# Performance work log

Measured on AMD Instinct MI355X. Metric: run time of the kernel, lower is better.

## Reference

```python
import jax, jax.numpy as jnp
import numpy as np

V, E, H, LM, LC = 50257, 512, 1024, 128, 256


def gru_cell(x, h, Wih, Whh, bih, bhh):
    # PyTorch nn.GRU cell, gate order (r, z, n)
    gi = x @ Wih.T + bih
    gh = h @ Whh.T + bhh
    i_r, i_z, i_n = jnp.split(gi, 3, -1)
    h_r, h_z, h_n = jnp.split(gh, 3, -1)
    r = jax.nn.sigmoid(i_r + h_r)
    z = jax.nn.sigmoid(i_z + h_z)
    n = jnp.tanh(i_n + r * h_n)
    return (1.0 - z) * n + z * h


def setup_inputs() -> dict:
    key = jax.random.key(0)
    ks = jax.random.split(key, 18)
    f = lambda k, sh: jax.random.normal(k, sh, jnp.float32) * 0.02
    return {
        "motion": jax.random.randint(ks[0], (1, LM), 0, V),
        "target_output": jax.random.randint(ks[1], (1, LC), 0, V),
        "enc_emb": f(ks[2], (V, E)),
        "enc_Wih": f(ks[3], (3 * H, E)),
        "enc_Whh": f(ks[4], (3 * H, H)),
        "enc_bih": f(ks[5], (3 * H,)),
        "enc_bhh": f(ks[6], (3 * H,)),
        "dec_emb": f(ks[7], (V, H)),
        "dec_Wih": f(ks[8], (3 * H, H)),
        "dec_Whh": f(ks[9], (3 * H, H)),
        "dec_bih": f(ks[10], (3 * H,)),
        "dec_bhh": f(ks[11], (3 * H,)),
        "attn_W": f(ks[12], (LM, 2 * H)),
        "attn_b": f(ks[13], (LM,)),
        "comb_W": f(ks[14], (H, 2 * H)),
        "comb_b": f(ks[15], (H,)),
        "out_W": f(ks[16], (V, H)),
        "out_b": f(ks[17], (V,)),
    }


def reference(motion, target_output, enc_emb, enc_Wih, enc_Whh, enc_bih, enc_bhh,
              dec_emb, dec_Wih, dec_Whh, dec_bih, dec_bhh,
              attn_W, attn_b, comb_W, comb_b, out_W, out_b):
    # ----- encode: per-step GRU over motion tokens (batch is hard-coded 1) -----
    toks = motion[0]  # [LM]

    def enc_step(h, t):
        h2 = gru_cell(enc_emb[t], h, enc_Wih, enc_Whh, enc_bih, enc_bhh)
        return h2, h2

    h0 = jnp.zeros((H,), jnp.float32)
    enc_h, enc_outs = jax.lax.scan(enc_step, h0, toks)  # enc_outs: [LM, H]

    # ----- decode with teacher forcing -----
    # original: decoder_input = SOS at idx 0, then target[idx-1] set at end of
    # step idx => step idx+1 consumes target[idx-1]; step 1 consumes target[-1].
    tgt = target_output[0]  # [LC]
    dec_in = jnp.concatenate([jnp.zeros((1,), tgt.dtype), tgt[-1:], tgt[:-2]])  # [LC]

    def dec_step(h, t):
        emb = dec_emb[t]  # [H] (dropout is identity at inference)
        attn_w = jax.nn.softmax(jnp.concatenate([emb, h]) @ attn_W.T + attn_b)  # [LM]
        ctx = attn_w @ enc_outs  # [H]
        x = jnp.concatenate([emb, ctx]) @ comb_W.T + comb_b  # [H] (no relu in source)
        h2 = gru_cell(x, h, dec_Wih, dec_Whh, dec_bih, dec_bhh)
        logp = jax.nn.log_softmax(h2 @ out_W.T + out_b)  # [V]
        return h2, logp

    _, logps = jax.lax.scan(dec_step, enc_h, dec_in)  # [LC, V]
    return logps[None]  # [1, LC, V] (permute(1,0,2) with batch=1)
```

## Files before the change

### kernel.cpp

```cpp
#include <hip/hip_runtime.h>

#define V_ 50257
#define E_ 512
#define H_ 1024
#define LM_ 128
#define LC_ 256
#define NBLK 256
#define ROWS 12
#define AREP 16
#define HREP 8
#define NT_OUT 786

typedef __attribute__((ext_vector_type(8))) short short8;
typedef __attribute__((ext_vector_type(4))) float f32x4;
typedef unsigned long long u64;

__device__ __forceinline__ unsigned short f2bf(float x) {
  union { float f; unsigned u; } v; v.f = x;
  unsigned r = v.u + 0x7fffu + ((v.u >> 16) & 1u);
  return (unsigned short)(r >> 16);
}
__device__ __forceinline__ float bflo(unsigned u) { union { unsigned u; float f; } v; v.u = u << 16; return v.f; }
__device__ __forceinline__ float bfhi(unsigned u) { union { unsigned u; float f; } v; v.u = u & 0xffff0000u; return v.f; }

__device__ __forceinline__ int grow4(int s, int i0) {
  return (s < 4) ? (i0 + s) : (s < 8) ? (1024 + i0 + (s - 4)) : (2048 + i0 + (s - 8));
}

__device__ __forceinline__ void st_u32(unsigned* p, unsigned v) {
  __hip_atomic_store(p, v, __ATOMIC_RELAXED, __HIP_MEMORY_SCOPE_AGENT);
}
__device__ __forceinline__ void st_u64(u64* p, u64 v) {
  __hip_atomic_store(p, v, __ATOMIC_RELAXED, __HIP_MEMORY_SCOPE_AGENT);
}
__device__ __forceinline__ u64 ld_u64(const u64* p) {
  return __hip_atomic_load(p, __ATOMIC_RELAXED, __HIP_MEMORY_SCOPE_AGENT);
}
__device__ __forceinline__ unsigned ld_u32(const unsigned* p) {
  return __hip_atomic_load(p, __ATOMIC_RELAXED, __HIP_MEMORY_SCOPE_AGENT);
}
__device__ __forceinline__ void atom_add_f32(float* p, float v) {
  (void)__hip_atomic_fetch_add(p, v, __ATOMIC_RELAXED, __HIP_MEMORY_SCOPE_AGENT);
}

__global__ void build_dec_tok(const int* __restrict__ tgt, int* __restrict__ dtok) {
  int t = threadIdx.x;
  dtok[t] = (t == 0) ? 0 : (t == 1 ? tgt[LC_ - 1] : tgt[t - 2]);
}

__global__ __launch_bounds__(256) void gemm_g(const float* __restrict__ A, int lda,
                                              const int* __restrict__ ridx,
                                              const float* __restrict__ B, int ldb,
                                              const float* __restrict__ bias,
                                              float* __restrict__ C, int ldc, int K) {
  __shared__ float As[16][68];
  __shared__ float Bs[16][68];
  const int bm = blockIdx.y * 64, bn = blockIdx.x * 64;
  const int tid = threadIdx.x;
  const int tx = tid & 15, ty = tid >> 4;
  const int lm = tid & 63, lk = (tid >> 6) * 4;
  const int arow = ridx ? ridx[bm + lm] : (bm + lm);
  const float* Arow = A + (size_t)arow * lda;
  float acc[4][4] = {};
  for (int k0 = 0; k0 < K; k0 += 16) {
    float4 av = *(const float4*)&Arow[k0 + lk];
    float4 bv = *(const float4*)&B[(size_t)(bn + lm) * ldb + k0 + lk];
    As[lk + 0][lm] = av.x; As[lk + 1][lm] = av.y; As[lk + 2][lm] = av.z; As[lk + 3][lm] = av.w;
    Bs[lk + 0][lm] = bv.x; Bs[lk + 1][lm] = bv.y; Bs[lk + 2][lm] = bv.z; Bs[lk + 3][lm] = bv.w;
    __syncthreads();
#pragma unroll
    for (int kk = 0; kk < 16; ++kk) {
      float4 a4 = *(const float4*)&As[kk][ty * 4];
      float4 b4 = *(const float4*)&Bs[kk][tx * 4];
      acc[0][0] += a4.x * b4.x; acc[0][1] += a4.x * b4.y; acc[0][2] += a4.x * b4.z; acc[0][3] += a4.x * b4.w;
      acc[1][0] += a4.y * b4.x; acc[1][1] += a4.y * b4.y; acc[1][2] += a4.y * b4.z; acc[1][3] += a4.y * b4.w;
      acc[2][0] += a4.z * b4.x; acc[2][1] += a4.z * b4.y; acc[2][2] += a4.z * b4.z; acc[2][3] += a4.z * b4.w;
      acc[3][0] += a4.w * b4.x; acc[3][1] += a4.w * b4.y; acc[3][2] += a4.w * b4.z; acc[3][3] += a4.w * b4.w;
    }
    __syncthreads();
  }
#pragma unroll
  for (int i = 0; i < 4; ++i) {
#pragma unroll
    for (int j = 0; j < 4; ++j) {
      int gm = bm + ty * 4 + i, gn = bn + tx * 4 + j;
      float bv = bias ? bias[gn] : 0.f;
      C[(size_t)gm * ldc + gn] = acc[i][j] + bv;
    }
  }
}

__global__ __launch_bounds__(256) void gemm_dual(const float* __restrict__ A, int lda,
                                                 const int* __restrict__ ridx,
                                                 const float* __restrict__ combW,
                                                 const float* __restrict__ comb_b,
                                                 const float* __restrict__ attnW,
                                                 const float* __restrict__ attn_b,
                                                 float* __restrict__ xE,
                                                 float* __restrict__ aE, int K) {
  __shared__ float As[16][68];
  __shared__ float Bs[16][68];
  const int bm = blockIdx.y * 64;
  const bool is_x = blockIdx.x < 16;
  const int bn = (is_x ? blockIdx.x : (blockIdx.x - 16)) * 64;
  const float* B = is_x ? combW : attnW;
  const int ldb = 2048;
  const float* bias = is_x ? comb_b : attn_b;
  float* C = is_x ? xE : aE;
  const int ldc = is_x ? 1024 : 128;
  const int tid = threadIdx.x;
  const int tx = tid & 15, ty = tid >> 4;
  const int lm = tid & 63, lk = (tid >> 6) * 4;
  const int arow = ridx[bm + lm];
  const float* Arow = A + (size_t)arow * lda;
  float acc[4][4] = {};
  for (int k0 = 0; k0 < K; k0 += 16) {
    float4 av = *(const float4*)&Arow[k0 + lk];
    float4 bv = *(const float4*)&B[(size_t)(bn + lm) * ldb + k0 + lk];
    As[lk + 0][lm] = av.x; As[lk + 1][lm] = av.y; As[lk + 2][lm] = av.z; As[lk + 3][lm] = av.w;
    Bs[lk + 0][lm] = bv.x; Bs[lk + 1][lm] = bv.y; Bs[lk + 2][lm] = bv.z; Bs[lk + 3][lm] = bv.w;
    __syncthreads();
#pragma unroll
    for (int kk = 0; kk < 16; ++kk) {
      float4 a4 = *(const float4*)&As[kk][ty * 4];
      float4 b4 = *(const float4*)&Bs[kk][tx * 4];
      acc[0][0] += a4.x * b4.x; acc[0][1] += a4.x * b4.y; acc[0][2] += a4.x * b4.z; acc[0][3] += a4.x * b4.w;
      acc[1][0] += a4.y * b4.x; acc[1][1] += a4.y * b4.y; acc[1][2] += a4.y * b4.z; acc[1][3] += a4.y * b4.w;
      acc[2][0] += a4.z * b4.x; acc[2][1] += a4.z * b4.y; acc[2][2] += a4.z * b4.z; acc[2][3] += a4.z * b4.w;
      acc[3][0] += a4.w * b4.x; acc[3][1] += a4.w * b4.y; acc[3][2] += a4.w * b4.z; acc[3][3] += a4.w * b4.w;
    }
    __syncthreads();
  }
#pragma unroll
  for (int i = 0; i < 4; ++i) {
#pragma unroll
    for (int j = 0; j < 4; ++j) {
      int gm = bm + ty * 4 + i, gn = bn + tx * 4 + j;
      C[(size_t)gm * ldc + gn] = acc[i][j] + bias[gn];
    }
  }
}

__global__ __launch_bounds__(256) void enc_rnn(const float* __restrict__ Whh,
                                               const float* __restrict__ bhh,
                                               const float* __restrict__ gi,
                                               u64* __restrict__ epk,
                                               float* __restrict__ outs) {
  __shared__ unsigned short Whl[ROWS][1024];
  __shared__ unsigned h_sh[512];
  __shared__ float h_own[4];
  __shared__ float bh[ROWS];
  __shared__ float ghl[ROWS];
  const int b = blockIdx.x, tid = threadIdx.x;
  const int w = tid >> 6, l = tid & 63;
  const int i0 = b * 4;
  const u64* myrep = epk + (size_t)(b & (HREP - 1)) * 1024;
  for (int idx = tid; idx < ROWS * 1024; idx += 256) {
    int s = idx >> 10, c = idx & 1023;
    Whl[s][c] = f2bf(Whh[(size_t)grow4(s, i0) * H_ + c]);
  }
  if (tid < ROWS) bh[tid] = bhh[grow4(tid, i0)];
  if (tid < 4) h_own[tid] = 0.f;
  __syncthreads();

  for (int t = 0; t < LM_; ++t) {
    float gr = 0.f, gz = 0.f, gn_ = 0.f;
    if (tid < 4) {
      const float* git = gi + (size_t)t * 3072;
      gr = git[i0 + tid]; gz = git[1024 + i0 + tid]; gn_ = git[2048 + i0 + tid];
    }
    if (t == 0) {
      h_sh[2 * tid] = 0u; h_sh[2 * tid + 1] = 0u;
    } else {
      const u64* pb = myrep + (size_t)(t & 1) * 512 + 2 * tid;
      const unsigned g = (unsigned)t;
      u64 q0, q1;
      for (;;) {
        q0 = ld_u64(pb); q1 = ld_u64(pb + 1);
        if ((unsigned)(q0 >> 32) == g && (unsigned)(q1 >> 32) == g) break;
        __builtin_amdgcn_s_sleep(1);
      }
      h_sh[2 * tid] = (unsigned)q0;
      h_sh[2 * tid + 1] = (unsigned)q1;
    }
    __syncthreads();

    for (int s = w; s < ROWS; s += 4) {
      float acc = 0.f;
#pragma unroll
      for (int e = 0; e < 8; ++e) {
        unsigned u = *(const unsigned*)&Whl[s][2 * (e * 64 + l)];
        unsigned hv = h_sh[e * 64 + l];
        acc += bflo(u) * bflo(hv) + bfhi(u) * bfhi(hv);
      }
#pragma unroll
      for (int off = 32; off; off >>= 1) acc += __shfl_xor(acc, off);
      if (l == 0) ghl[s] = acc;
    }
    __syncthreads();
    if (tid < 4) {
      int i = tid, ig = i0 + i;
      float hr = ghl[i] + bh[i], hz = ghl[4 + i] + bh[4 + i], hn = ghl[8 + i] + bh[8 + i];
      float r = 1.f / (1.f + expf(-(gr + hr)));
      float z = 1.f / (1.f + expf(-(gz + hz)));
      float n = tanhf(gn_ + r * hn);
      float hpv = (1.f - z) * n + z * h_own[i];
      h_own[i] = hpv;
      float v0 = __shfl(hpv, 0), v1 = __shfl(hpv, 1);
      float v2 = __shfl(hpv, 2), v3 = __shfl(hpv, 3);
      if (tid == 0) {
        u64 gg = (u64)(unsigned)(t + 1) << 32;
        u64 p0 = gg | (u64)((unsigned)f2bf(v0) | ((unsigned)f2bf(v1) << 16));
        u64 p1 = gg | (u64)((unsigned)f2bf(v2) | ((unsigned)f2bf(v3) << 16));
        size_t slot = (size_t)((t + 1) & 1) * 512 + 2 * b;
#pragma unroll
        for (int r2 = 0; r2 < HREP; ++r2) {
          st_u64(epk + (size_t)r2 * 1024 + slot, p0);
          st_u64(epk + (size_t)r2 * 1024 + slot + 1, p1);
        }
      }
      outs[(size_t)t * H_ + ig] = hpv;
    }
  }
}

__global__ __launch_bounds__(256) void dec_rnn(const float* __restrict__ Whh,
                                               const float* __restrict__ bhh,
                                               const float* __restrict__ attn_W,
                                               const float* __restrict__ G,
                                               const float* __restrict__ P1,
                                               const float* __restrict__ aE,
                                               const float* __restrict__ hfin,
                                               float* __restrict__ a_acc,
                                               u64* __restrict__ dpk,
                                               unsigned* __restrict__ dflags,
                                               unsigned short* __restrict__ Hs) {
  __shared__ unsigned short Whl[ROWS][1024];
  __shared__ unsigned Ac[2 * 128];
  __shared__ float Gl[ROWS][128];
  __shared__ unsigned h_sh[512];
  __shared__ float a_f[128];
  __shared__ float h_own[4];
  __shared__ float bh[ROWS];
  __shared__ float ghl[ROWS];
  __shared__ float giS[ROWS];
  const int b = blockIdx.x, tid = threadIdx.x;
  const int w = tid >> 6, l = tid & 63;
  const int i0 = b * 4;
  for (int idx = tid; idx < ROWS * 1024; idx += 256) {
    int s = idx >> 10, c = idx & 1023;
    Whl[s][c] = f2bf(Whh[(size_t)grow4(s, i0) * H_ + c]);
  }
  if (tid < 256) {
    int u = tid >> 7, j = tid & 127;
    float2 wv = *(const float2*)&attn_W[(size_t)j * 2048 + 1024 + i0 + 2 * u];
    Ac[tid] = (unsigned)f2bf(wv.x) | ((unsigned)f2bf(wv.y) << 16);
  }
  for (int idx = tid; idx < ROWS * 128; idx += 256) {
    int s = idx >> 7, c = idx & 127;
    Gl[s][c] = G[(size_t)grow4(s, i0) * 128 + c];
  }
  if (tid < ROWS) bh[tid] = bhh[grow4(tid, i0)];
  if (tid < 4) h_own[tid] = hfin[i0 + tid];
  __syncthreads();

  {
    float h0 = h_own[0], h1 = h_own[1], h2 = h_own[2], h3 = h_own[3];
    if (tid < 128) {
      unsigned w0 = Ac[tid], w1 = Ac[128 + tid];
      float a0 = bflo(w0) * h0 + bfhi(w0) * h1 + bflo(w1) * h2 + bfhi(w1) * h3;
      atom_add_f32(&a_acc[(b & (AREP - 1)) * 128 + tid], a0);
    }
    __syncthreads();
    if (tid == 0) st_u32(&dflags[b * 16], 1u);
  }

  for (int t = 0; t < LC_; ++t) {
    u64 aacc[16]; u64 aEv = 0;
    if (tid < 64) {
      const unsigned need = (unsigned)(t + 1);
      for (;;) {
        unsigned f0 = ld_u32(&dflags[tid * 16]);
        unsigned f1 = ld_u32(&dflags[(tid + 64) * 16]);
        unsigned f2 = ld_u32(&dflags[(tid + 128) * 16]);
        unsigned f3 = ld_u32(&dflags[(tid + 192) * 16]);
        unsigned mn = min(min(f0, f1), min(f2, f3));
        if (__all((int)(mn >= need))) break;
        __builtin_amdgcn_s_sleep(1);
      }
      const u64* ab = (const u64*)(a_acc + (size_t)t * (AREP * 128)) + l;
#pragma unroll
      for (int r = 0; r < AREP; ++r) aacc[r] = ld_u64(ab + r * 64);
      float2 ae2 = *(const float2*)&aE[(size_t)t * LM_ + 2 * l];
      aEv = ((u64)__float_as_uint(ae2.y) << 32) | (u64)__float_as_uint(ae2.x);
    }
    float p1p[3];
    if (l == 0) {
#pragma unroll
      for (int k = 0; k < 3; ++k) p1p[k] = P1[(size_t)t * 3072 + grow4(w + 4 * k, i0)];
    } else {
      p1p[0] = p1p[1] = p1p[2] = 0.f;
    }
    if (t == 0) {
      float4 hv = ((const float4*)hfin)[tid];
      h_sh[2 * tid] = (unsigned)f2bf(hv.x) | ((unsigned)f2bf(hv.y) << 16);
      h_sh[2 * tid + 1] = (unsigned)f2bf(hv.z) | ((unsigned)f2bf(hv.w) << 16);
    } else {
      const u64* pb = dpk + (size_t)(t & 1) * 512 + 2 * tid;
      const unsigned g = (unsigned)t;
      u64 q0, q1;
      for (;;) {
        q0 = ld_u64(pb); q1 = ld_u64(pb + 1);
        if ((unsigned)(q0 >> 32) == g && (unsigned)(q1 >> 32) == g) break;
        __builtin_amdgcn_s_sleep(1);
      }
      h_sh[2 * tid] = (unsigned)q0;
      h_sh[2 * tid + 1] = (unsigned)q1;
    }
    __syncthreads();

    if (tid < 64) {
      float s0 = 0.f, s1 = 0.f;
#pragma unroll
      for (int r = 0; r < AREP; ++r) {
        s0 += __uint_as_float((unsigned)aacc[r]);
        s1 += __uint_as_float((unsigned)(aacc[r] >> 32));
      }
      a_f[2 * l] = s0 + __uint_as_float((unsigned)aEv);
      a_f[2 * l + 1] = s1 + __uint_as_float((unsigned)(aEv >> 32));
    }
    for (int s = w; s < ROWS; s += 4) {
      float acc = 0.f;
#pragma unroll
      for (int e = 0; e < 8; ++e) {
        unsigned u = *(const unsigned*)&Whl[s][2 * (e * 64 + l)];
        unsigned hv = h_sh[e * 64 + l];
        acc += bflo(u) * bflo(hv) + bfhi(u) * bfhi(hv);
      }
#pragma unroll
      for (int off = 32; off; off >>= 1) acc += __shfl_xor(acc, off);
      if (l == 0) ghl[s] = acc;
    }
    __syncthreads();

    float ax = a_f[2 * l], ay = a_f[2 * l + 1];
    float mx = fmaxf(ax, ay);
#pragma unroll
    for (int off = 32; off; off >>= 1) mx = fmaxf(mx, __shfl_xor(mx, off));
    float pe0 = expf(ax - mx), pe1 = expf(ay - mx);
    float zs = pe0 + pe1;
#pragma unroll
    for (int off = 32; off; off >>= 1) zs += __shfl_xor(zs, off);
    float w0 = pe0 / zs, w1 = pe1 / zs;
#pragma unroll
    for (int k = 0; k < 3; ++k) {
      int s = w + 4 * k;
      float2 g2 = *(const float2*)&Gl[s][2 * l];
      float acc = g2.x * w0 + g2.y * w1;
#pragma unroll
      for (int off = 32; off; off >>= 1) acc += __shfl_xor(acc, off);
      if (l == 0) giS[s] = acc + p1p[k];
    }
    __syncthreads();

    if (tid < 4) {
      int i = tid, ig = i0 + i;
      float hr = ghl[i] + bh[i], hz = ghl[4 + i] + bh[4 + i], hn = ghl[8 + i] + bh[8 + i];
      float r = 1.f / (1.f + expf(-(giS[i] + hr)));
      float z = 1.f / (1.f + expf(-(giS[4 + i] + hz)));
      float n = tanhf(giS[8 + i] + r * hn);
      float hpv = (1.f - z) * n + z * h_own[i];
      h_own[i] = hpv;
      float v0 = __shfl(hpv, 0), v1 = __shfl(hpv, 1);
      float v2 = __shfl(hpv, 2), v3 = __shfl(hpv, 3);
      if (tid == 0 && t < LC_ - 1) {
        u64 gg = (u64)(unsigned)(t + 1) << 32;
        u64* pb = dpk + (size_t)((t + 1) & 1) * 512 + 2 * b;
        st_u64(pb,     gg | (u64)((unsigned)f2bf(v0) | ((unsigned)f2bf(v1) << 16)));
        st_u64(pb + 1, gg | (u64)((unsigned)f2bf(v2) | ((unsigned)f2bf(v3) << 16)));
      }
      Hs[(size_t)t * H_ + ig] = f2bf(hpv);
    }
    __syncthreads();

    if (t < LC_ - 1) {
      float h0 = h_own[0], h1 = h_own[1], h2 = h_own[2], h3 = h_own[3];
      if (tid < 128) {
        unsigned w0p = Ac[tid], w1p = Ac[128 + tid];
        float a0 = bflo(w0p) * h0 + bfhi(w0p) * h1 + bflo(w1p) * h2 + bfhi(w1p) * h3;
        atom_add_f32(&a_acc[(size_t)(t + 1) * (AREP * 128) + (b & (AREP - 1)) * 128 + tid], a0);
      }
    }
    __syncthreads();
    if (tid == 0) st_u32(&dflags[b * 16], (unsigned)(t + 2));
  }
}

__global__ __launch_bounds__(256) void out_gemm(const unsigned short* __restrict__ A,
                                                const float* __restrict__ Wf, int ldw,
                                                const float* __restrict__ bias,
                                                float* __restrict__ C,
                                                float* __restrict__ pmax,
                                                float* __restrict__ psum,
                                                int N, int K) {
  __shared__ unsigned short As[2][256][40];
  __shared__ unsigned short Bs[2][64][40];
  const int bn = blockIdx.x * 64, bx = blockIdx.x;
  const int tid = threadIdx.x, w = tid >> 6, l = tid & 63;
  const int NIT = K / 32;
  f32x4 acc[4][4];
#pragma unroll
  for (int mf = 0; mf < 4; ++mf)
#pragma unroll
    for (int nf = 0; nf < 4; ++nf) acc[mf][nf] = (f32x4){0.f, 0.f, 0.f, 0.f};

  const int bn_r0 = (tid) >> 3, bkc0 = tid & 7;
  const int bn_r1 = (tid + 256) >> 3, bkc1 = (tid + 256) & 7;

  short8 ar[4];
  float4 fv[2];
  {
    const unsigned short* src = A + (size_t)tid * K;
#pragma unroll
    for (int kc = 0; kc < 4; ++kc) ar[kc] = *(const short8*)(src + kc * 8);
    int gn0 = bn + bn_r0, gn1 = bn + bn_r1;
    fv[0] = (gn0 < N) ? *(const float4*)&Wf[(size_t)gn0 * ldw + bkc0 * 4] : (float4){0, 0, 0, 0};
    fv[1] = (gn1 < N) ? *(const float4*)&Wf[(size_t)gn1 * ldw + bkc1 * 4] : (float4){0, 0, 0, 0};
#pragma unroll
    for (int kc = 0; kc < 4; ++kc) *(short8*)&As[0][tid][kc * 8] = ar[kc];
    uint2 p0, p1;
    p0.x = (unsigned)f2bf(fv[0].x) | ((unsigned)f2bf(fv[0].y) << 16);
    p0.y = (unsigned)f2bf(fv[0].z) | ((unsigned)f2bf(fv[0].w) << 16);
    p1.x = (unsigned)f2bf(fv[1].x) | ((unsigned)f2bf(fv[1].y) << 16);
    p1.y = (unsigned)f2bf(fv[1].z) | ((unsigned)f2bf(fv[1].w) << 16);
    *(uint2*)&Bs[0][bn_r0][bkc0 * 4] = p0;
    *(uint2*)&Bs[0][bn_r1][bkc1 * 4] = p1;
  }

  for (int it = 0; it < NIT; ++it) {
    const int cur = it & 1, nxt = cur ^ 1;
    __syncthreads();
    if (it + 1 < NIT) {
      int k0n = (it + 1) * 32;
      const unsigned short* src = A + (size_t)tid * K + k0n;
#pragma unroll
      for (int kc = 0; kc < 4; ++kc) ar[kc] = *(const short8*)(src + kc * 8);
      int gn0 = bn + bn_r0, gn1 = bn + bn_r1;
      fv[0] = (gn0 < N) ? *(const float4*)&Wf[(size_t)gn0 * ldw + k0n + bkc0 * 4] : (float4){0, 0, 0, 0};
      fv[1] = (gn1 < N) ? *(const float4*)&Wf[(size_t)gn1 * ldw + k0n + bkc1 * 4] : (float4){0, 0, 0, 0};
    }
    const int k8 = (l >> 4) * 8;
    short8 af4[4], bf4[4];
#pragma unroll
    for (int mf = 0; mf < 4; ++mf) af4[mf] = *(const short8*)&As[cur][w * 64 + mf * 16 + (l & 15)][k8];
#pragma unroll
    for (int nf = 0; nf < 4; ++nf) bf4[nf] = *(const short8*)&Bs[cur][nf * 16 + (l & 15)][k8];
#pragma unroll
    for (int mf = 0; mf < 4; ++mf)
#pragma unroll
      for (int nf = 0; nf < 4; ++nf)
        acc[mf][nf] = __builtin_amdgcn_mfma_f32_16x16x32_bf16(af4[mf], bf4[nf], acc[mf][nf], 0, 0, 0);
    if (it + 1 < NIT) {
#pragma unroll
      for (int kc = 0; kc < 4; ++kc) *(short8*)&As[nxt][tid][kc * 8] = ar[kc];
      uint2 p0, p1;
      p0.x = (unsigned)f2bf(fv[0].x) | ((unsigned)f2bf(fv[0].y) << 16);
      p0.y = (unsigned)f2bf(fv[0].z) | ((unsigned)f2bf(fv[0].w) << 16);
      p1.x = (unsigned)f2bf(fv[1].x) | ((unsigned)f2bf(fv[1].y) << 16);
      p1.y = (unsigned)f2bf(fv[1].z) | ((unsigned)f2bf(fv[1].w) << 16);
      *(uint2*)&Bs[nxt][bn_r0][bkc0 * 4] = p0;
      *(uint2*)&Bs[nxt][bn_r1][bkc1 * 4] = p1;
    }
  }
#pragma unroll
  for (int mf = 0; mf < 4; ++mf) {
#pragma unroll
    for (int i = 0; i < 4; ++i) {
      int m = w * 64 + mf * 16 + (l >> 4) * 4 + i;
      float v[4];
#pragma unroll
      for (int nf = 0; nf < 4; ++nf) {
        int n = bn + nf * 16 + (l & 15);
        float val = -3.4e38f;
        if (n < N) {
          val = acc[mf][nf][i] + bias[n];
          C[(size_t)m * N + n] = val;
        }
        v[nf] = val;
      }
      float mv = fmaxf(fmaxf(v[0], v[1]), fmaxf(v[2], v[3]));
#pragma unroll
      for (int off = 1; off < 16; off <<= 1) mv = fmaxf(mv, __shfl_xor(mv, off));
      float se = 0.f;
#pragma unroll
      for (int nf = 0; nf < 4; ++nf) se += (v[nf] > -1e38f) ? expf(v[nf] - mv) : 0.f;
#pragma unroll
      for (int off = 1; off < 16; off <<= 1) se += __shfl_xor(se, off);
      if ((l & 15) == 0) {
        pmax[(size_t)m * NT_OUT + bx] = mv;
        psum[(size_t)m * NT_OUT + bx] = se;
      }
    }
  }
}

__global__ __launch_bounds__(256) void lsm_combine(const float* __restrict__ pmax,
                                                   const float* __restrict__ psum,
                                                   float* __restrict__ stats) {
  const int r = blockIdx.x, tid = threadIdx.x, w = tid >> 6, l = tid & 63;
  __shared__ float red[4];
  __shared__ float Msh;
  const float* pm = pmax + (size_t)r * NT_OUT;
  const float* ps = psum + (size_t)r * NT_OUT;
  float m = -3.4e38f;
  for (int j = tid; j < NT_OUT; j += 256) m = fmaxf(m, pm[j]);
#pragma unroll
  for (int off = 32; off; off >>= 1) m = fmaxf(m, __shfl_xor(m, off));
  if (l == 0) red[w] = m;
  __syncthreads();
  if (tid == 0) Msh = fmaxf(fmaxf(red[0], red[1]), fmaxf(red[2], red[3]));
  __syncthreads();
  float M = Msh;
  float s = 0.f;
  for (int j = tid; j < NT_OUT; j += 256) s += ps[j] * expf(pm[j] - M);
#pragma unroll
  for (int off = 32; off; off >>= 1) s += __shfl_xor(s, off);
  if (l == 0) red[w] = s;
  __syncthreads();
  if (tid == 0) {
    stats[r] = M;
    stats[256 + r] = logf(red[0] + red[1] + red[2] + red[3]);
  }
}

__global__ __launch_bounds__(256) void lsm_apply(float* __restrict__ C, const float* __restrict__ stats, int N) {
  int r = blockIdx.y;
  int ci = blockIdx.x * 256 + threadIdx.x;
  if (ci < N) {
    size_t idx = (size_t)r * N + ci;
    C[idx] = C[idx] - stats[r] - stats[256 + r];
  }
}

extern "C" void kernel_launch(void* const* d_in, const int* in_sizes, int n_in,
                              void* d_out, int out_size, void* d_ws, size_t ws_size,
                              hipStream_t stream) {
  (void)in_sizes; (void)n_in; (void)out_size; (void)ws_size;
  const int* motion = (const int*)d_in[0];
  const int* tgt = (const int*)d_in[1];
  const float* enc_emb = (const float*)d_in[2];
  const float* enc_Wih = (const float*)d_in[3];
  const float* enc_Whh = (const float*)d_in[4];
  const float* enc_bih = (const float*)d_in[5];
  const float* enc_bhh = (const float*)d_in[6];
  const float* dec_emb = (const float*)d_in[7];
  const float* dec_Wih = (const float*)d_in[8];
  const float* dec_Whh = (const float*)d_in[9];
  const float* dec_bih = (const float*)d_in[10];
  const float* dec_bhh = (const float*)d_in[11];
  const float* attn_W = (const float*)d_in[12];
  const float* attn_b = (const float*)d_in[13];
  const float* comb_W = (const float*)d_in[14];
  const float* comb_b = (const float*)d_in[15];
  const float* out_W = (const float*)d_in[16];
  const float* out_b = (const float*)d_in[17];
  float* out = (float*)d_out;

  float* wsf = (float*)d_ws;
  size_t o = 0;
  auto F = [&](size_t n) { float* p = wsf + o; o += (n + 3) & ~(size_t)3; return p; };
  float* enc_gi = F(128 * 3072);
  float* enc_outs = F(128 * 1024);
  float* aE = F(256 * 128);
  float* xE = F(256 * 1024);
  float* P1 = F(256 * 3072);
  float* M2T = F(128 * 1024);
  float* Gm = F(3072 * 128);
  int* dec_tok = (int*)F(256);
  u64* epk = (u64*)F(HREP * 2048);
  u64* dpk = (u64*)F(2048);
  unsigned* dflags = (unsigned*)F(4096);
  float* a_acc = F(LC_ * AREP * 128);
  float* stats = F(512);
  float* pmax = F(256 * NT_OUT);
  float* psum = F(256 * NT_OUT);
  unsigned short* Hs = (unsigned short*)F(256 * 1024 / 2);

  hipMemsetAsync(epk, 0, (HREP * 2048 + 2048 + 4096 + LC_ * AREP * 128) * sizeof(float), stream);

  build_dec_tok<<<1, 256, 0, stream>>>(tgt, dec_tok);
  gemm_g<<<dim3(48, 2), 256, 0, stream>>>(enc_emb, 512, motion, enc_Wih, 512, enc_bih, enc_gi, 3072, 512);
  gemm_dual<<<dim3(18, 4), 256, 0, stream>>>(dec_emb, 1024, dec_tok, comb_W, comb_b, attn_W, attn_b, xE, aE, 1024);
  gemm_g<<<dim3(48, 4), 256, 0, stream>>>(xE, 1024, nullptr, dec_Wih, 1024, dec_bih, P1, 3072, 1024);

  enc_rnn<<<NBLK, 256, 0, stream>>>(enc_Whh, enc_bhh, enc_gi, epk, enc_outs);

  gemm_g<<<dim3(16, 2), 256, 0, stream>>>(enc_outs, 1024, nullptr, comb_W + 1024, 2048, nullptr, M2T, 1024, 1024);
  gemm_g<<<dim3(2, 48), 256, 0, stream>>>(dec_Wih, 1024, nullptr, M2T, 1024, nullptr, Gm, 128, 1024);

  dec_rnn<<<NBLK, 256, 0, stream>>>(dec_Whh, dec_bhh, attn_W, Gm, P1, aE,
                                    enc_outs + (size_t)(LM_ - 1) * H_, a_acc, dpk, dflags, Hs);

  out_gemm<<<NT_OUT, 256, 0, stream>>>(Hs, out_W, 1024, out_b, out, pmax, psum, V_, 1024);
  lsm_combine<<<256, 256, 0, stream>>>(pmax, psum, stats);
  lsm_apply<<<dim3(197, 256), 256, 0, stream>>>(out, stats, V_);
}
```

Before: 2.208 ms.

## Fuse decoder recurrence and output GEMM into one persistent launch

Merges the decoder RNN kernel and the vocabulary projection GEMM into a single launch. The extra blocks first touch out_W rows to warm the L2 cache while the recurrence runs, then spin on per-block done flags before computing two output tiles each. This removes a kernel launch boundary and overlaps weight prefetch with the serial recurrence. It relies on all 256 RNN blocks being co-resident with the waiting blocks, which risks deadlock or fewer resources for the RNN if the spinners get scheduled first.

```diff
diff --git a/kernel.cpp b/kernel.cpp
--- a/kernel.cpp
+++ b/kernel.cpp
@@ -10,6 +10,8 @@
 #define AREP 16
 #define HREP 8
 #define NT_OUT 786
+#define NOB 393
+#define DONEF (LC_ + 1)
 
 typedef __attribute__((ext_vector_type(8))) short short8;
 typedef __attribute__((ext_vector_type(4))) float f32x4;
@@ -224,7 +226,23 @@
   }
 }
 
-__global__ __launch_bounds__(256) void dec_rnn(const float* __restrict__ Whh,
+struct DecS {
+  unsigned short Whl[ROWS][1024];
+  unsigned Ac[256];
+  float Gl[ROWS][128];
+  unsigned h_sh[512];
+  float a_f[128];
+  float h_own[4];
+  float bh[ROWS];
+  float ghl[ROWS];
+  float giS[ROWS];
+};
+struct OutS {
+  unsigned short As[2][256][40];
+  unsigned short Bs[2][64][40];
+};
+
+__global__ __launch_bounds__(256) void dec_out(const float* __restrict__ Whh,
                                                const float* __restrict__ bhh,
                                                const float* __restrict__ attn_W,
                                                const float* __restrict__ G,
@@ -234,272 +252,298 @@
                                                float* __restrict__ a_acc,
                                                u64* __restrict__ dpk,
                                                unsigned* __restrict__ dflags,
-                                               unsigned short* __restrict__ Hs) {
-  __shared__ unsigned short Whl[ROWS][1024];
-  __shared__ unsigned Ac[2 * 128];
-  __shared__ float Gl[ROWS][128];
-  __shared__ unsigned h_sh[512];
-  __shared__ float a_f[128];
-  __shared__ float h_own[4];
-  __shared__ float bh[ROWS];
-  __shared__ float ghl[ROWS];
-  __shared__ float giS[ROWS];
-  const int b = blockIdx.x, tid = threadIdx.x;
-  const int w = tid >> 6, l = tid & 63;
-  const int i0 = b * 4;
-  for (int idx = tid; idx < ROWS * 1024; idx += 256) {
-    int s = idx >> 10, c = idx & 1023;
-    Whl[s][c] = f2bf(Whh[(size_t)grow4(s, i0) * H_ + c]);
-  }
-  if (tid < 256) {
-    int u = tid >> 7, j = tid & 127;
-    float2 wv = *(const float2*)&attn_W[(size_t)j * 2048 + 1024 + i0 + 2 * u];
-    Ac[tid] = (unsigned)f2bf(wv.x) | ((unsigned)f2bf(wv.y) << 16);
-  }
-  for (int idx = tid; idx < ROWS * 128; idx += 256) {
-    int s = idx >> 7, c = idx & 127;
-    Gl[s][c] = G[(size_t)grow4(s, i0) * 128 + c];
-  }
-  if (tid < ROWS) bh[tid] = bhh[grow4(tid, i0)];
-  if (tid < 4) h_own[tid] = hfin[i0 + tid];
-  __syncthreads();
-
-  {
-    float h0 = h_own[0], h1 = h_own[1], h2 = h_own[2], h3 = h_own[3];
-    if (tid < 128) {
-      unsigned w0 = Ac[tid], w1 = Ac[128 + tid];
-      float a0 = bflo(w0) * h0 + bfhi(w0) * h1 + bflo(w1) * h2 + bfhi(w1) * h3;
-      atom_add_f32(&a_acc[(b & (AREP - 1)) * 128 + tid], a0);
-    }
-    __syncthreads();
-    if (tid == 0) st_u32(&dflags[b * 16], 1u);
-  }
-
-  for (int t = 0; t < LC_; ++t) {
-    u64 aacc[16]; u64 aEv = 0;
+                                               unsigned short* __restrict__ Hs,
+                                               const float* __restrict__ Wf, int ldw,
+                                               const float* __restrict__ obias,
+                                               float* __restrict__ C,
+                                               float* __restrict__ pmax,
+                                               float* __restrict__ psum,
+                                               int N, int K) {
+  __shared__ alignas(16) char smraw[sizeof(OutS)];
+  const int tid = threadIdx.x, w = tid >> 6, l = tid & 63;
+
+  if (blockIdx.x < NBLK) {
+    DecS& S = *(DecS*)smraw;
+    const int b = blockIdx.x;
+    const int i0 = b * 4;
+    for (int idx = tid; idx < ROWS * 1024; idx += 256) {
+      int s = idx >> 10, c = idx & 1023;
+      S.Whl[s][c] = f2bf(Whh[(size_t)grow4(s, i0) * H_ + c]);
+    }
+    {
+      int u = tid >> 7, j = tid & 127;
+      float2 wv = *(const float2*)&attn_W[(size_t)j * 2048 + 1024 + i0 + 2 * u];
+      S.Ac[tid] = (unsigned)f2bf(wv.x) | ((unsigned)f2bf(wv.y) << 16);
+    }
+    for (int idx = tid; idx < ROWS * 128; idx += 256) {
+      int s = idx >> 7, c = idx & 127;
+      S.Gl[s][c] = G[(size_t)grow4(s, i0) * 128 + c];
+    }
+    if (tid < ROWS) S.bh[tid] = bhh[grow4(tid, i0)];
+    if (tid < 4) S.h_own[tid] = hfin[i0 + tid];
+    __syncthreads();
+
+    {
+      float h0 = S.h_own[0], h1 = S.h_own[1], h2 = S.h_own[2], h3 = S.h_own[3];
+      if (tid < 128) {
+        unsigned w0 = S.Ac[tid], w1 = S.Ac[128 + tid];
+        float a0 = bflo(w0) * h0 + bfhi(w0) * h1 + bflo(w1) * h2 + bfhi(w1) * h3;
+        atom_add_f32(&a_acc[(b & (AREP - 1)) * 128 + tid], a0);
+      }
+      __syncthreads();
+      if (tid == 0) st_u32(&dflags[b * 16], 1u);
+    }
+
+    for (int t = 0; t < LC_; ++t) {
+      u64 aacc[16]; u64 aEv = 0;
+      if (tid < 64) {
+        const unsigned need = (unsigned)(t + 1);
+        for (;;) {
+          unsigned f0 = ld_u32(&dflags[tid * 16]);
+          unsigned f1 = ld_u32(&dflags[(tid + 64) * 16]);
+          unsigned f2 = ld_u32(&dflags[(tid + 128) * 16]);
+          unsigned f3 = ld_u32(&dflags[(tid + 192) * 16]);
+          unsigned mn = min(min(f0, f1), min(f2, f3));
+          if (__all((int)(mn >= need))) break;
+          __builtin_amdgcn_s_sleep(1);
+        }
+        const u64* ab = (const u64*)(a_acc + (size_t)t * (AREP * 128)) + l;
+#pragma unroll
+        for (int r = 0; r < AREP; ++r) aacc[r] = ld_u64(ab + r * 64);
+        float2 ae2 = *(const float2*)&aE[(size_t)t * LM_ + 2 * l];
+        aEv = ((u64)__float_as_uint(ae2.y) << 32) | (u64)__float_as_uint(ae2.x);
+      }
+      float p1p[3];
+      if (l == 0) {
+#pragma unroll
+        for (int k = 0; k < 3; ++k) p1p[k] = P1[(size_t)t * 3072 + grow4(w + 4 * k, i0)];
+      } else {
+        p1p[0] = p1p[1] = p1p[2] = 0.f;
+      }
+      if (t == 0) {
+        float4 hv = ((const float4*)hfin)[tid];
+        S.h_sh[2 * tid] = (unsigned)f2bf(hv.x) | ((unsigned)f2bf(hv.y) << 16);
+        S.h_sh[2 * tid + 1] = (unsigned)f2bf(hv.z) | ((unsigned)f2bf(hv.w) << 16);
+      } else {
+        const u64* pb = dpk + (size_t)(t & 1) * 512 + 2 * tid;
+        const unsigned g = (unsigned)t;
+        u64 q0, q1;
+        for (;;) {
+          q0 = ld_u64(pb); q1 = ld_u64(pb + 1);
+          if ((unsigned)(q0 >> 32) == g && (unsigned)(q1 >> 32) == g) break;
+          __builtin_amdgcn_s_sleep(1);
+        }
+        S.h_sh[2 * tid] = (unsigned)q0;
+        S.h_sh[2 * tid + 1] = (unsigned)q1;
+      }
+      __syncthreads();
+
+      if (tid < 64) {
+        float s0 = 0.f, s1 = 0.f;
+#pragma unroll
+        for (int r = 0; r < AREP; ++r) {
+          s0 += __uint_as_float((unsigned)aacc[r]);
+          s1 += __uint_as_float((unsigned)(aacc[r] >> 32));
+        }
+        S.a_f[2 * l] = s0 + __uint_as_float((unsigned)aEv);
+        S.a_f[2 * l + 1] = s1 + __uint_as_float((unsigned)(aEv >> 32));
+      }
+      for (int s = w; s < ROWS; s += 4) {
+        float acc = 0.f;
+#pragma unroll
+        for (int e = 0; e < 8; ++e) {
+          unsigned u = *(const unsigned*)&S.Whl[s][2 * (e * 64 + l)];
+          unsigned hv = S.h_sh[e * 64 + l];
+          acc += bflo(u) * bflo(hv) + bfhi(u) * bfhi(hv);
+        }
+#pragma unroll
+        for (int off = 32; off; off >>= 1) acc += __shfl_xor(acc, off);
+        if (l == 0) S.ghl[s] = acc;
+      }
+      __syncthreads();
+
+      float ax = S.a_f[2 * l], ay = S.a_f[2 * l + 1];
+      float mx = fmaxf(ax, ay);
+#pragma unroll
+      for (int off = 32; off; off >>= 1) mx = fmaxf(mx, __shfl_xor(mx, off));
+      float pe0 = expf(ax - mx), pe1 = expf(ay - mx);
+      float zs = pe0 + pe1;
+#pragma unroll
+      for (int off = 32; off; off >>= 1) zs += __shfl_xor(zs, off);
+      float w0 = pe0 / zs, w1 = pe1 / zs;
+#pragma unroll
+      for (int k = 0; k < 3; ++k) {
+        int s = w + 4 * k;
+        float2 g2 = *(const float2*)&S.Gl[s][2 * l];
+        float acc = g2.x * w0 + g2.y * w1;
+#pragma unroll
+        for (int off = 32; off; off >>= 1) acc += __shfl_xor(acc, off);
+        if (l == 0) S.giS[s] = acc + p1p[k];
+      }
+      __syncthreads();
+
+      if (tid < 4) {
+        int i = tid, ig = i0 + i;
+        float hr = S.ghl[i] + S.bh[i], hz = S.ghl[4 + i] + S.bh[4 + i], hn = S.ghl[8 + i] + S.bh[8 + i];
+        float r = 1.f / (1.f + expf(-(S.giS[i] + hr)));
+        float z = 1.f / (1.f + expf(-(S.giS[4 + i] + hz)));
+        float n = tanhf(S.giS[8 + i] + r * hn);
+        float hpv = (1.f - z) * n + z * S.h_own[i];
+        S.h_own[i] = hpv;
+        float v0 = __shfl(hpv, 0), v1 = __shfl(hpv, 1);
+        float v2 = __shfl(hpv, 2), v3 = __shfl(hpv, 3);
+        if (tid == 0 && t < LC_ - 1) {
+          u64 gg = (u64)(unsigned)(t + 1) << 32;
+          u64* pb = dpk + (size_t)((t + 1) & 1) * 512 + 2 * b;
+          st_u64(pb,     gg | (u64)((unsigned)f2bf(v0) | ((unsigned)f2bf(v1) << 16)));
+          st_u64(pb + 1, gg | (u64)((unsigned)f2bf(v2) | ((unsigned)f2bf(v3) << 16)));
+        }
+        Hs[(size_t)t * H_ + ig] = f2bf(hpv);
+      }
+      __syncthreads();
+
+      if (t < LC_ - 1) {
+        float h0 = S.h_own[0], h1 = S.h_own[1], h2 = S.h_own[2], h3 = S.h_own[3];
+        if (tid < 128) {
+          unsigned w0p = S.Ac[tid], w1p = S.Ac[128 + tid];
+          float a0 = bflo(w0p) * h0 + bfhi(w0p) * h1 + bflo(w1p) * h2 + bfhi(w1p) * h3;
+          atom_add_f32(&a_acc[(size_t)(t + 1) * (AREP * 128) + (b & (AREP - 1)) * 128 + tid], a0);
+        }
+      }
+      __syncthreads();
+      if (tid == 0 && t < LC_ - 1) st_u32(&dflags[b * 16], (unsigned)(t + 2));
+    }
+    __syncthreads();
+    if (tid == 0) {
+      __builtin_amdgcn_fence(__ATOMIC_RELEASE, "agent");
+      st_u32(&dflags[b * 16], (unsigned)DONEF);
+    }
+  } else {
+    OutS& O = *(OutS*)smraw;
+    const int ob = blockIdx.x - NBLK;
+
+    {
+      float acc = 0.f;
+      const float4* W4 = (const float4*)Wf;
+      const int ld4 = ldw >> 2;
+      for (int i = tid; i < 128 * 256; i += 256) {
+        int row = i >> 8, c4 = i & 255;
+        int gn = (2 * ob + (row >> 6)) * 64 + (row & 63);
+        if (gn < N) acc += W4[(size_t)gn * ld4 + c4].x;
+      }
+      asm volatile("" :: "v"(acc));
+    }
     if (tid < 64) {
-      const unsigned need = (unsigned)(t + 1);
       for (;;) {
         unsigned f0 = ld_u32(&dflags[tid * 16]);
         unsigned f1 = ld_u32(&dflags[(tid + 64) * 16]);
         unsigned f2 = ld_u32(&dflags[(tid + 128) * 16]);
         unsigned f3 = ld_u32(&dflags[(tid + 192) * 16]);
         unsigned mn = min(min(f0, f1), min(f2, f3));
-        if (__all((int)(mn >= need))) break;
-        __builtin_amdgcn_s_sleep(1);
-      }
-      const u64* ab = (const u64*)(a_acc + (size_t)t * (AREP * 128)) + l;
-#pragma unroll
-      for (int r = 0; r < AREP; ++r) aacc[r] = ld_u64(ab + r * 64);
-      float2 ae2 = *(const float2*)&aE[(size_t)t * LM_ + 2 * l];
-      aEv = ((u64)__float_as_uint(ae2.y) << 32) | (u64)__float_as_uint(ae2.x);
-    }
-    float p1p[3];
-    if (l == 0) {
-#pragma unroll
-      for (int k = 0; k < 3; ++k) p1p[k] = P1[(size_t)t * 3072 + grow4(w + 4 * k, i0)];
-    } else {
-      p1p[0] = p1p[1] = p1p[2] = 0.f;
-    }
-    if (t == 0) {
-      float4 hv = ((const float4*)hfin)[tid];
-      h_sh[2 * tid] = (unsigned)f2bf(hv.x) | ((unsigned)f2bf(hv.y) << 16);
-      h_sh[2 * tid + 1] = (unsigned)f2bf(hv.z) | ((unsigned)f2bf(hv.w) << 16);
-    } else {
-      const u64* pb = dpk + (size_t)(t & 1) * 512 + 2 * tid;
-      const unsigned g = (unsigned)t;
-      u64 q0, q1;
-      for (;;) {
-        q0 = ld_u64(pb); q1 = ld_u64(pb + 1);
-        if ((unsigned)(q0 >> 32) == g && (unsigned)(q1 >> 32) == g) break;
-        __builtin_amdgcn_s_sleep(1);
-      }
-      h_sh[2 * tid] = (unsigned)q0;
-      h_sh[2 * tid + 1] = (unsigned)q1;
-    }
-    __syncthreads();
-
-    if (tid < 64) {
-      float s0 = 0.f, s1 = 0.f;
-#pragma unroll
-      for (int r = 0; r < AREP; ++r) {
-        s0 += __uint_as_float((unsigned)aacc[r]);
-        s1 += __uint_as_float((unsigned)(aacc[r] >> 32));
-      }
-      a_f[2 * l] = s0 + __uint_as_float((unsigned)aEv);
-      a_f[2 * l + 1] = s1 + __uint_as_float((unsigned)(aEv >> 32));
-    }
-    for (int s = w; s < ROWS; s += 4) {
-      float acc = 0.f;
-#pragma unroll
-      for (int e = 0; e < 8; ++e) {
-        unsigned u = *(const unsigned*)&Whl[s][2 * (e * 64 + l)];
-        unsigned hv = h_sh[e * 64 + l];
-        acc += bflo(u) * bflo(hv) + bfhi(u) * bfhi(hv);
-      }
-#pragma unroll
-      for (int off = 32; off; off >>= 1) acc += __shfl_xor(acc, off);
-      if (l == 0) ghl[s] = acc;
-    }
-    __syncthreads();
-
-    float ax = a_f[2 * l], ay = a_f[2 * l + 1];
-    float mx = fmaxf(ax, ay);
-#pragma unroll
-    for (int off = 32; off; off >>= 1) mx = fmaxf(mx, __shfl_xor(mx, off));
-    float pe0 = expf(ax - mx), pe1 = expf(ay - mx);
-    float zs = pe0 + pe1;
-#pragma unroll
-    for (int off = 32; off; off >>= 1) zs += __shfl_xor(zs, off);
-    float w0 = pe0 / zs, w1 = pe1 / zs;
-#pragma unroll
-    for (int k = 0; k < 3; ++k) {
-      int s = w + 4 * k;
-      float2 g2 = *(const float2*)&Gl[s][2 * l];
-      float acc = g2.x * w0 + g2.y * w1;
-#pragma unroll
-      for (int off = 32; off; off >>= 1) acc += __shfl_xor(acc, off);
-      if (l == 0) giS[s] = acc + p1p[k];
-    }
-    __syncthreads();
-
-    if (tid < 4) {
-      int i = tid, ig = i0 + i;
-      float hr = ghl[i] + bh[i], hz = ghl[4 + i] + bh[4 + i], hn = ghl[8 + i] + bh[8 + i];
-      float r = 1.f / (1.f + expf(-(giS[i] + hr)));
-      float z = 1.f / (1.f + expf(-(giS[4 + i] + hz)));
-      float n = tanhf(giS[8 + i] + r * hn);
-      float hpv = (1.f - z) * n + z * h_own[i];
-      h_own[i] = hpv;
-      float v0 = __shfl(hpv, 0), v1 = __shfl(hpv, 1);
-      float v2 = __shfl(hpv, 2), v3 = __shfl(hpv, 3);
-      if (tid == 0 && t < LC_ - 1) {
-        u64 gg = (u64)(unsigned)(t + 1) << 32;
-        u64* pb = dpk + (size_t)((t + 1) & 1) * 512 + 2 * b;
-        st_u64(pb,     gg | (u64)((unsigned)f2bf(v0) | ((unsigned)f2bf(v1) << 16)));
-        st_u64(pb + 1, gg | (u64)((unsigned)f2bf(v2) | ((unsigned)f2bf(v3) << 16)));
-      }
-      Hs[(size_t)t * H_ + ig] = f2bf(hpv);
-    }
-    __syncthreads();
-
-    if (t < LC_ - 1) {
-      float h0 = h_own[0], h1 = h_own[1], h2 = h_own[2], h3 = h_own[3];
-      if (tid < 128) {
-        unsigned w0p = Ac[tid], w1p = Ac[128 + tid];
-        float a0 = bflo(w0p) * h0 + bfhi(w0p) * h1 + bflo(w1p) * h2 + bfhi(w1p) * h3;
-        atom_add_f32(&a_acc[(size_t)(t + 1) * (AREP * 128) + (b & (AREP - 1)) * 128 + tid], a0);
-      }
-    }
-    __syncthreads();
-    if (tid == 0) st_u32(&dflags[b * 16], (unsigned)(t + 2));
-  }
-}
-
-__global__ __launch_bounds__(256) void out_gemm(const unsigned short* __restrict__ A,
-                                                const float* __restrict__ Wf, int ldw,
-                                                const float* __restrict__ bias,
-                                                float* __restrict__ C,
-                                                float* __restrict__ pmax,
-                                                float* __restrict__ psum,
-                                                int N, int K) {
-  __shared__ unsigned short As[2][256][40];
-  __shared__ unsigned short Bs[2][64][40];
-  const int bn = blockIdx.x * 64, bx = blockIdx.x;
-  const int tid = threadIdx.x, w = tid >> 6, l = tid & 63;
-  const int NIT = K / 32;
-  f32x4 acc[4][4];
-#pragma unroll
-  for (int mf = 0; mf < 4; ++mf)
-#pragma unroll
-    for (int nf = 0; nf < 4; ++nf) acc[mf][nf] = (f32x4){0.f, 0.f, 0.f, 0.f};
-
-  const int bn_r0 = (tid) >> 3, bkc0 = tid & 7;
-  const int bn_r1 = (tid + 256) >> 3, bkc1 = (tid + 256) & 7;
-
-  short8 ar[4];
-  float4 fv[2];
-  {
-    const unsigned short* src = A + (size_t)tid * K;
-#pragma unroll
-    for (int kc = 0; kc < 4; ++kc) ar[kc] = *(const short8*)(src + kc * 8);
-    int gn0 = bn + bn_r0, gn1 = bn + bn_r1;
-    fv[0] = (gn0 < N) ? *(const float4*)&Wf[(size_t)gn0 * ldw + bkc0 * 4] : (float4){0, 0, 0, 0};
-    fv[1] = (gn1 < N) ? *(const float4*)&Wf[(size_t)gn1 * ldw + bkc1 * 4] : (float4){0, 0, 0, 0};
-#pragma unroll
-    for (int kc = 0; kc < 4; ++kc) *(short8*)&As[0][tid][kc * 8] = ar[kc];
-    uint2 p0, p1;
-    p0.x = (unsigned)f2bf(fv[0].x) | ((unsigned)f2bf(fv[0].y) << 16);
-    p0.y = (unsigned)f2bf(fv[0].z) | ((unsigned)f2bf(fv[0].w) << 16);
-    p1.x = (unsigned)f2bf(fv[1].x) | ((unsigned)f2bf(fv[1].y) << 16);
-    p1.y = (unsigned)f2bf(fv[1].z) | ((unsigned)f2bf(fv[1].w) << 16);
-    *(uint2*)&Bs[0][bn_r0][bkc0 * 4] = p0;
-    *(uint2*)&Bs[0][bn_r1][bkc1 * 4] = p1;
-  }
-
-  for (int it = 0; it < NIT; ++it) {
-    const int cur = it & 1, nxt = cur ^ 1;
-    __syncthreads();
-    if (it + 1 < NIT) {
-      int k0n = (it + 1) * 32;
-      const unsigned short* src = A + (size_t)tid * K + k0n;
-#pragma unroll
-      for (int kc = 0; kc < 4; ++kc) ar[kc] = *(const short8*)(src + kc * 8);
-      int gn0 = bn + bn_r0, gn1 = bn + bn_r1;
-      fv[0] = (gn0 < N) ? *(const float4*)&Wf[(size_t)gn0 * ldw + k0n + bkc0 * 4] : (float4){0, 0, 0, 0};
-      fv[1] = (gn1 < N) ? *(const float4*)&Wf[(size_t)gn1 * ldw + k0n + bkc1 * 4] : (float4){0, 0, 0, 0};
-    }
-    const int k8 = (l >> 4) * 8;
-    short8 af4[4], bf4[4];
-#pragma unroll
-    for (int mf = 0; mf < 4; ++mf) af4[mf] = *(const short8*)&As[cur][w * 64 + mf * 16 + (l & 15)][k8];
-#pragma unroll
-    for (int nf = 0; nf < 4; ++nf) bf4[nf] = *(const short8*)&Bs[cur][nf * 16 + (l & 15)][k8];
-#pragma unroll
-    for (int mf = 0; mf < 4; ++mf)
-#pragma unroll
-      for (int nf = 0; nf < 4; ++nf)
-        acc[mf][nf] = __builtin_amdgcn_mfma_f32_16x16x32_bf16(af4[mf], bf4[nf], acc[mf][nf], 0, 0, 0);
-    if (it + 1 < NIT) {
-#pragma unroll
-      for (int kc = 0; kc < 4; ++kc) *(short8*)&As[nxt][tid][kc * 8] = ar[kc];
-      uint2 p0, p1;
-      p0.x = (unsigned)f2bf(fv[0].x) | ((unsigned)f2bf(fv[0].y) << 16);
-      p0.y = (unsigned)f2bf(fv[0].z) | ((unsigned)f2bf(fv[0].w) << 16);
-      p1.x = (unsigned)f2bf(fv[1].x) | ((unsigned)f2bf(fv[1].y) << 16);
-      p1.y = (unsigned)f2bf(fv[1].z) | ((unsigned)f2bf(fv[1].w) << 16);
-      *(uint2*)&Bs[nxt][bn_r0][bkc0 * 4] = p0;
-      *(uint2*)&Bs[nxt][bn_r1][bkc1 * 4] = p1;
-    }
-  }
-#pragma unroll
-  for (int mf = 0; mf < 4; ++mf) {
-#pragma unroll
-    for (int i = 0; i < 4; ++i) {
-      int m = w * 64 + mf * 16 + (l >> 4) * 4 + i;
-      float v[4];
-#pragma unroll
-      for (int nf = 0; nf < 4; ++nf) {
-        int n = bn + nf * 16 + (l & 15);
-        float val = -3.4e38f;
-        if (n < N) {
-          val = acc[mf][nf][i] + bias[n];
-          C[(size_t)m * N + n] = val;
-        }
-        v[nf] = val;
-      }
-      float mv = fmaxf(fmaxf(v[0], v[1]), fmaxf(v[2], v[3]));
-#pragma unroll
-      for (int off = 1; off < 16; off <<= 1) mv = fmaxf(mv, __shfl_xor(mv, off));
-      float se = 0.f;
-#pragma unroll
-      for (int nf = 0; nf < 4; ++nf) se += (v[nf] > -1e38f) ? expf(v[nf] - mv) : 0.f;
-#pragma unroll
-      for (int off = 1; off < 16; off <<= 1) se += __shfl_xor(se, off);
-      if ((l & 15) == 0) {
-        pmax[(size_t)m * NT_OUT + bx] = mv;
-        psum[(size_t)m * NT_OUT + bx] = se;
-      }
+        if (__all((int)(mn >= (unsigned)DONEF))) break;
+        __builtin_amdgcn_s_sleep(64);
+      }
+    }
+    __syncthreads();
+    __builtin_amdgcn_fence(__ATOMIC_ACQUIRE, "agent");
+    __syncthreads();
+
+    const int bn_r0 = tid >> 3, bkc0 = tid & 7;
+    const int bn_r1 = (tid + 256) >> 3, bkc1 = (tid + 256) & 7;
+    for (int tt = 0; tt < 2; ++tt) {
+      const int bx = 2 * ob + tt, bn = bx * 64;
+      const int NIT = K / 32;
+      f32x4 acc[4][4];
+#pragma unroll
+      for (int mf = 0; mf < 4; ++mf)
+#pragma unroll
+        for (int nf = 0; nf < 4; ++nf) acc[mf][nf] = (f32x4){0.f, 0.f, 0.f, 0.f};
+
+      short8 ar[4];
+      float4 fv[2];
+      {
+        const unsigned short* src = Hs + (size_t)tid * K;
+#pragma unroll
+        for (int kc = 0; kc < 4; ++kc) ar[kc] = *(const short8*)(src + kc * 8);
+        int gn0 = bn + bn_r0, gn1 = bn + bn_r1;
+        fv[0] = (gn0 < N) ? *(const float4*)&Wf[(size_t)gn0 * ldw + bkc0 * 4] : (float4){0, 0, 0, 0};
+        fv[1] = (gn1 < N) ? *(const float4*)&Wf[(size_t)gn1 * ldw + bkc1 * 4] : (float4){0, 0, 0, 0};
+#pragma unroll
+        for (int kc = 0; kc < 4; ++kc) *(short8*)&O.As[0][tid][kc * 8] = ar[kc];
+        uint2 p0, p1;
+        p0.x = (unsigned)f2bf(fv[0].x) | ((unsigned)f2bf(fv[0].y) << 16);
+        p0.y = (unsigned)f2bf(fv[0].z) | ((unsigned)f2bf(fv[0].w) << 16);
+        p1.x = (unsigned)f2bf(fv[1].x) | ((unsigned)f2bf(fv[1].y) << 16);
+        p1.y = (unsigned)f2bf(fv[1].z) | ((unsigned)f2bf(fv[1].w) << 16);
+        *(uint2*)&O.Bs[0][bn_r0][bkc0 * 4] = p0;
+        *(uint2*)&O.Bs[0][bn_r1][bkc1 * 4] = p1;
+      }
+      for (int it = 0; it < NIT; ++it) {
+        const int cur = it & 1, nxt = cur ^ 1;
+        __syncthreads();
+        if (it + 1 < NIT) {
+          int k0n = (it + 1) * 32;
+          const unsigned short* src = Hs + (size_t)tid * K + k0n;
+#pragma unroll
+          for (int kc = 0; kc < 4; ++kc) ar[kc] = *(const short8*)(src + kc * 8);
+          int gn0 = bn + bn_r0, gn1 = bn + bn_r1;
+          fv[0] = (gn0 < N) ? *(const float4*)&Wf[(size_t)gn0 * ldw + k0n + bkc0 * 4] : (float4){0, 0, 0, 0};
+          fv[1] = (gn1 < N) ? *(const float4*)&Wf[(size_t)gn1 * ldw + k0n + bkc1 * 4] : (float4){0, 0, 0, 0};
+        }
+        const int k8 = (l >> 4) * 8;
+        short8 af4[4], bf4[4];
+#pragma unroll
+        for (int mf = 0; mf < 4; ++mf) af4[mf] = *(const short8*)&O.As[cur][w * 64 + mf * 16 + (l & 15)][k8];
+#pragma unroll
+        for (int nf = 0; nf < 4; ++nf) bf4[nf] = *(const short8*)&O.Bs[cur][nf * 16 + (l & 15)][k8];
+#pragma unroll
+        for (int mf = 0; mf < 4; ++mf)
+#pragma unroll
+          for (int nf = 0; nf < 4; ++nf)
+            acc[mf][nf] = __builtin_amdgcn_mfma_f32_16x16x32_bf16(af4[mf], bf4[nf], acc[mf][nf], 0, 0, 0);
+        if (it + 1 < NIT) {
+#pragma unroll
+          for (int kc = 0; kc < 4; ++kc) *(short8*)&O.As[nxt][tid][kc * 8] = ar[kc];
+          uint2 p0, p1;
+          p0.x = (unsigned)f2bf(fv[0].x) | ((unsigned)f2bf(fv[0].y) << 16);
+          p0.y = (unsigned)f2bf(fv[0].z) | ((unsigned)f2bf(fv[0].w) << 16);
+          p1.x = (unsigned)f2bf(fv[1].x) | ((unsigned)f2bf(fv[1].y) << 16);
+          p1.y = (unsigned)f2bf(fv[1].z) | ((unsigned)f2bf(fv[1].w) << 16);
+          *(uint2*)&O.Bs[nxt][bn_r0][bkc0 * 4] = p0;
+          *(uint2*)&O.Bs[nxt][bn_r1][bkc1 * 4] = p1;
+        }
+      }
+#pragma unroll
+      for (int mf = 0; mf < 4; ++mf) {
+#pragma unroll
+        for (int i = 0; i < 4; ++i) {
+          int m = w * 64 + mf * 16 + (l >> 4) * 4 + i;
+          float v[4];
+#pragma unroll
+          for (int nf = 0; nf < 4; ++nf) {
+            int n = bn + nf * 16 + (l & 15);
+            float val = -3.4e38f;
+            if (n < N) {
+              val = acc[mf][nf][i] + obias[n];
+              C[(size_t)m * N + n] = val;
+            }
+            v[nf] = val;
+          }
+          float mv = fmaxf(fmaxf(v[0], v[1]), fmaxf(v[2], v[3]));
+#pragma unroll
+          for (int off = 1; off < 16; off <<= 1) mv = fmaxf(mv, __shfl_xor(mv, off));
+          float se = 0.f;
+#pragma unroll
+          for (int nf = 0; nf < 4; ++nf) se += (v[nf] > -1e38f) ? expf(v[nf] - mv) : 0.f;
+#pragma unroll
+          for (int off = 1; off < 16; off <<= 1) se += __shfl_xor(se, off);
+          if ((l & 15) == 0) {
+            pmax[(size_t)m * NT_OUT + bx] = mv;
+            psum[(size_t)m * NT_OUT + bx] = se;
+          }
+        }
+      }
+      __syncthreads();
     }
   }
 }
@@ -598,10 +642,10 @@
   gemm_g<<<dim3(16, 2), 256, 0, stream>>>(enc_outs, 1024, nullptr, comb_W + 1024, 2048, nullptr, M2T, 1024, 1024);
   gemm_g<<<dim3(2, 48), 256, 0, stream>>>(dec_Wih, 1024, nullptr, M2T, 1024, nullptr, Gm, 128, 1024);
 
-  dec_rnn<<<NBLK, 256, 0, stream>>>(dec_Whh, dec_bhh, attn_W, Gm, P1, aE,
-                                    enc_outs + (size_t)(LM_ - 1) * H_, a_acc, dpk, dflags, Hs);
-
-  out_gemm<<<NT_OUT, 256, 0, stream>>>(Hs, out_W, 1024, out_b, out, pmax, psum, V_, 1024);
+  dec_out<<<NBLK + NOB, 256, 0, stream>>>(dec_Whh, dec_bhh, attn_W, Gm, P1, aE,
+                                          enc_outs + (size_t)(LM_ - 1) * H_, a_acc, dpk, dflags, Hs,
+                                          out_W, 1024, out_b, out, pmax, psum, V_, 1024);
+
   lsm_combine<<<256, 256, 0, stream>>>(pmax, psum, stats);
   lsm_apply<<<dim3(197, 256), 256, 0, stream>>>(out, stats, V_);
 }
```

Measured after the change: 2.358 ms. +6.8%, slower.
